# Optimization experiments

Measured on AMD Instinct MI355X. Metric: run time of the kernel, lower is better.

The kernel has to match this reference:

```python
import jax, jax.numpy as jnp
import numpy as np

DIM = 256
WIN = 4
HEADS = 4
HEAD_DIM = DIM // HEADS
SCALE = HEAD_DIM ** (-0.5)


def setup_inputs() -> dict:
    key = jax.random.key(0)
    k1, k2, k3 = jax.random.split(key, 3)
    x = jax.random.normal(k1, (4, DIM, 32, 32, 32), dtype=jnp.float32)
    # xavier_uniform with gain=0.02 ~ small weights; scale approximated
    w_qkv = jax.random.normal(k2, (3 * DIM, DIM), dtype=jnp.float32) * 0.02
    w_proj = jax.random.normal(k3, (DIM, DIM), dtype=jnp.float32) * 0.02
    return {"x": x, "w_qkv": w_qkv, "w_proj": w_proj}


def reference(x, w_qkv, w_proj):
    B, C, D, H, W = x.shape
    N = D * H * W
    s = round(N ** (1.0 / 3.0))  # perfect cube asserted by original module
    w = WIN
    # (B,C,D,H,W) -> (B,N,C) -> (B,s,s,s,C)
    xt = x.reshape(B, C, N).transpose(0, 2, 1).reshape(B, s, s, s, C)
    pad = (w - s % w) % w
    if pad:
        xt = jnp.pad(xt, ((0, 0), (0, pad), (0, pad), (0, pad), (0, 0)))
    Sp = s + pad
    n = Sp // w  # windows per axis
    # torch unfold layout: (B, nD, nH, nW, C, w, w, w)
    xw = xt.reshape(B, n, w, n, w, n, w, C).transpose(0, 1, 3, 5, 7, 2, 4, 6)
    # faithful to torch .view(-1, w*w*w, C): row-major reinterpret of (C,w,w,w)
    xw = xw.reshape(-1, w * w * w, C)  # (nw, 64, C)
    nw, ntok = xw.shape[0], xw.shape[1]
    qkv = (xw @ w_qkv.T).reshape(nw, ntok, 3, HEADS, HEAD_DIM)
    q, k, v = qkv[:, :, 0], qkv[:, :, 1], qkv[:, :, 2]  # (nw, ntok, heads, hd)
    # faithful: NO head permute in original -> attention over the heads axis
    attn = jnp.einsum('wnhd,wngd->wnhg', q, k) * SCALE  # (nw, ntok, heads, heads)
    attn = jnp.clip(attn, -10.0, 10.0)
    attn = jax.nn.softmax(attn, axis=-1)
    out = jnp.einsum('wnhg,wngd->wnhd', attn, v)  # (nw, ntok, heads, hd)
    # faithful torch transpose(1,2).reshape(nw, ntok, dim)
    out = out.transpose(0, 2, 1, 3).reshape(nw, ntok, C)
    out = out @ w_proj.T
    out = out.reshape(B, n, n, n, w, w, w, C)
    out = out.transpose(0, 1, 4, 2, 5, 3, 6, 7).reshape(B, Sp, Sp, Sp, C)
    out = out[:, :s, :s, :s, :].transpose(0, 4, 1, 2, 3)  # (B,C,s,s,s)
    return out
```

## Files before the change

### kernel.cpp

```cpp
#include <hip/hip_runtime.h>

typedef _Float16 f16;
typedef f16 f16x2 __attribute__((ext_vector_type(2)));
typedef f16 f16x4 __attribute__((ext_vector_type(4)));
typedef f16 f16x8 __attribute__((ext_vector_type(8)));
typedef float f32x4 __attribute__((ext_vector_type(4)));

union v8split { f16x8 v8; f16x2 v2[4]; };

#define WQF_OFF 0
#define WPF_OFF (768 * 256 * 2)
#define XW_OFF  (WPF_OFF + 256 * 256 * 2)
#define O2_OFF  (XW_OFF + (size_t)2048 * 16384 * 2)
#define WS_NEED (O2_OFF + (size_t)2048 * 16384 * 2)

#define QKV_LDS_OFF 32768
#define SMEM_TOTAL 131072

__global__ __launch_bounds__(256) void cvt_weights_frag_k(
    const float* __restrict__ wq, const float* __restrict__ wp,
    f16* __restrict__ wq_f, f16* __restrict__ wp_f) {
  int tid2 = blockIdx.x * 256 + threadIdx.x;
  if (tid2 < 24576) {
    const int lane = tid2 & 63, kt = (tid2 >> 6) & 7, f0 = tid2 >> 9;
    const float* s = wq + (size_t)(f0 * 16 + (lane & 15)) * 256 + kt * 32 + (lane >> 4) * 8;
    f16* d = wq_f + (size_t)tid2 * 8;
#pragma unroll
    for (int e = 0; e < 8; ++e) d[e] = (f16)s[e];
  } else if (tid2 < 32768) {
    const int t2 = tid2 - 24576;
    const int lane = t2 & 63, kt = (t2 >> 6) & 7, f0 = t2 >> 9;
    const float* s = wp + (size_t)(f0 * 16 + (lane & 15)) * 256 + kt * 32 + (lane >> 4) * 8;
    f16* d = wp_f + (size_t)t2 * 8;
#pragma unroll
    for (int e = 0; e < 8; ++e) d[e] = (f16)s[e];
  }
}

__device__ __forceinline__ char* xwp(char* s, int row, int colbyte) {
  return s + row * 512 + (colbyte ^ (((row ^ (row >> 3)) & 7) << 4));
}
__device__ __forceinline__ char* qvp(char* s, int t, int fbyte) {
  return s + QKV_LDS_OFF + t * 1536 + (fbyte ^ ((t & 7) << 4));
}

__device__ __forceinline__ float qswap1f(float v) {
  int x = __builtin_bit_cast(int, v);
  x = __builtin_amdgcn_update_dpp(0, x, 0xB1, 0xf, 0xf, true);
  return __builtin_bit_cast(float, x);
}
__device__ __forceinline__ float qswap2f(float v) {
  int x = __builtin_bit_cast(int, v);
  x = __builtin_amdgcn_update_dpp(0, x, 0x4E, 0xf, 0xf, true);
  return __builtin_bit_cast(float, x);
}

#if __has_builtin(__builtin_amdgcn_fdot2)
__device__ __forceinline__ float fdot2f(f16x2 a, f16x2 b, float c) {
  return __builtin_amdgcn_fdot2(a, b, c, false);
}
#else
__device__ __forceinline__ float fdot2f(f16x2 a, f16x2 b, float c) {
  return c + (float)a[0] * (float)b[0] + (float)a[1] * (float)b[1];
}
#endif

__global__ __launch_bounds__(256) void gather_k(const float* __restrict__ x,
                                                f16* __restrict__ xw_all) {
  const int g = blockIdx.x >> 4, cb = blockIdx.x & 15;
  const int b = g >> 6, iw = (g >> 3) & 7, jw = g & 7;
  const int tid = threadIdx.x;
  const int c = cb * 16 + (tid >> 4), a = (tid >> 2) & 3, bb = tid & 3;
  const float* src = x + (size_t)b * 8388608 + (size_t)c * 32768 +
                     (iw * 4 + a) * 1024 + (jw * 4 + bb) * 32;
  const int t = c >> 2;
  const int c2b = (c & 3) * 128 + a * 32 + bb * 8;
  const int byt = t * 512 + (c2b ^ (((t ^ (t >> 3)) & 7) << 4));
  char* wbase = (char*)(xw_all + (size_t)(g << 3) * 16384) + byt;
#pragma unroll
  for (int kw = 0; kw < 8; ++kw) {
    float4 v = *(const float4*)(src + kw * 4);
    f16x4 h;
    h[0] = (f16)v.x; h[1] = (f16)v.y; h[2] = (f16)v.z; h[3] = (f16)v.w;
    *(f16x4*)(wbase + kw * 32768) = h;
  }
}

__global__ __launch_bounds__(1024) void win_attn_k(
    const f16* __restrict__ xw_all, const f16* __restrict__ wq_f,
    const f16* __restrict__ wp_f, f16* __restrict__ o2T) {
  extern __shared__ char smem[];
  const int wi = blockIdx.x;
  const int tid = threadIdx.x, wv = tid >> 6, lane = tid & 63;
  const int lcol = lane & 15, lq = lane >> 4;

  {
    const char* g = (const char*)(xw_all + (size_t)wi * 16384) + tid * 16;
    __builtin_amdgcn_global_load_lds(
        (const __attribute__((address_space(1))) void*)(g),
        (__attribute__((address_space(3))) void*)(smem + tid * 16), 16, 0, 0);
    __builtin_amdgcn_global_load_lds(
        (const __attribute__((address_space(1))) void*)(g + 16384),
        (__attribute__((address_space(3))) void*)(smem + tid * 16 + 16384), 16, 0, 0);
  }
  __syncthreads();

  {
    f32x4 acc[3][4] = {};
    const f16* wbase = wq_f + ((size_t)wv * 3 * 8 + 0) * 64 * 8 + lane * 8;
#pragma unroll
    for (int kt = 0; kt < 8; ++kt) {
      f16x8 bf[4];
#pragma unroll
      for (int nt = 0; nt < 4; ++nt)
        bf[nt] = *(const f16x8*)xwp(smem, nt * 16 + lcol, kt * 64 + lq * 16);
#pragma unroll
      for (int ms = 0; ms < 3; ++ms) {
        f16x8 af = *(const f16x8*)(wbase + (size_t)(ms * 8 + kt) * 512);
#pragma unroll
        for (int nt = 0; nt < 4; ++nt)
          acc[ms][nt] = __builtin_amdgcn_mfma_f32_16x16x32_f16(af, bf[nt], acc[ms][nt], 0, 0, 0);
      }
    }
    const int fs = wv * 48;
#pragma unroll
    for (int ms = 0; ms < 3; ++ms)
#pragma unroll
      for (int nt = 0; nt < 4; ++nt) {
        f16x4 hv;
        hv[0] = (f16)acc[ms][nt][0]; hv[1] = (f16)acc[ms][nt][1];
        hv[2] = (f16)acc[ms][nt][2]; hv[3] = (f16)acc[ms][nt][3];
        *(f16x4*)qvp(smem, nt * 16 + lcol, (fs + ms * 16 + lq * 4) * 2) = hv;
      }
  }
  __syncthreads();

  {
    const int tt = lane >> 4, h = (lane >> 2) & 3, dq = lane & 3;
    const int t = wv * 4 + tt;
    const int db = dq * 32;

    f16x2 q2[8];
#pragma unroll
    for (int j = 0; j < 2; ++j) {
      v8split u;
      u.v8 = *(const f16x8*)qvp(smem, t, h * 128 + db + j * 16);
      q2[j * 4 + 0] = u.v2[0]; q2[j * 4 + 1] = u.v2[1];
      q2[j * 4 + 2] = u.v2[2]; q2[j * 4 + 3] = u.v2[3];
    }
    float s[4];
#pragma unroll
    for (int g = 0; g < 4; ++g) {
      float a = 0.f;
#pragma unroll
      for (int j = 0; j < 2; ++j) {
        v8split u;
        u.v8 = *(const f16x8*)qvp(smem, t, 512 + g * 128 + db + j * 16);
        a = fdot2f(q2[j * 4 + 0], u.v2[0], a);
        a = fdot2f(q2[j * 4 + 1], u.v2[1], a);
        a = fdot2f(q2[j * 4 + 2], u.v2[2], a);
        a = fdot2f(q2[j * 4 + 3], u.v2[3], a);
      }
      s[g] = a;
    }
#pragma unroll
    for (int g = 0; g < 4; ++g) {
      s[g] += qswap1f(s[g]);
      s[g] += qswap2f(s[g]);
    }

    float mx = -1e30f;
#pragma unroll
    for (int g = 0; g < 4; ++g) {
      float v = fminf(fmaxf(s[g] * 0.125f, -10.f), 10.f);
      s[g] = v; mx = fmaxf(mx, v);
    }
    float sum = 0.f;
#pragma unroll
    for (int g = 0; g < 4; ++g) { s[g] = __expf(s[g] - mx); sum += s[g]; }
    float inv = 1.f / sum;
#pragma unroll
    for (int g = 0; g < 4; ++g) s[g] *= inv;

    float o[16] = {};
#pragma unroll
    for (int g = 0; g < 4; ++g) {
      float p = s[g];
#pragma unroll
      for (int j = 0; j < 2; ++j) {
        v8split u;
        u.v8 = *(const f16x8*)qvp(smem, t, 1024 + g * 128 + db + j * 16);
#pragma unroll
        for (int i = 0; i < 4; ++i) {
          o[j * 8 + 2 * i]     += p * (float)u.v2[i][0];
          o[j * 8 + 2 * i + 1] += p * (float)u.v2[i][1];
        }
      }
    }
    const int row = h * 16 + (t >> 2);
    const int cb0 = (t & 3) * 128 + db;
#pragma unroll
    for (int j = 0; j < 2; ++j) {
      f16x8 ov;
      ov[0] = (f16)o[j * 8 + 0]; ov[1] = (f16)o[j * 8 + 1];
      ov[2] = (f16)o[j * 8 + 2]; ov[3] = (f16)o[j * 8 + 3];
      ov[4] = (f16)o[j * 8 + 4]; ov[5] = (f16)o[j * 8 + 5];
      ov[6] = (f16)o[j * 8 + 6]; ov[7] = (f16)o[j * 8 + 7];
      *(f16x8*)xwp(smem, row, cb0 + j * 16) = ov;
    }
  }
  __syncthreads();

  {
    f32x4 acc2[4] = {};
    const int c3 = wv * 16 + lcol;
    const f16* bp = wp_f + ((size_t)wv * 8) * 64 * 8 + lane * 8;
#pragma unroll
    for (int kt = 0; kt < 8; ++kt) {
      f16x8 bfr = *(const f16x8*)(bp + (size_t)kt * 512);
#pragma unroll
      for (int mt = 0; mt < 4; ++mt) {
        f16x8 afr = *(const f16x8*)xwp(smem, mt * 16 + lcol, kt * 64 + lq * 16);
        acc2[mt] = __builtin_amdgcn_mfma_f32_16x16x32_f16(afr, bfr, acc2[mt], 0, 0, 0);
      }
    }
    f16* ob = o2T + (size_t)wi * 16384;
#pragma unroll
    for (int mt = 0; mt < 4; ++mt) {
      f16x4 hv;
      hv[0] = (f16)acc2[mt][0]; hv[1] = (f16)acc2[mt][1];
      hv[2] = (f16)acc2[mt][2]; hv[3] = (f16)acc2[mt][3];
      *(f16x4*)(ob + c3 * 64 + mt * 16 + lq * 4) = hv;
    }
  }
}

__global__ __launch_bounds__(256) void scatter_k(const f16* __restrict__ o2T,
                                                 float* __restrict__ out) {
  const int g = blockIdx.x >> 4, cb = blockIdx.x & 15;
  const int b = g >> 6, iw = (g >> 3) & 7, jw = g & 7;
  const int tid = threadIdx.x;
  const int c3 = cb * 16 + (tid >> 4), a = (tid >> 2) & 3, bb = tid & 3;
  const f16* rbase = o2T + (size_t)(g << 3) * 16384 + c3 * 64 + a * 16 + bb * 4;
  float* dst = out + (size_t)b * 8388608 + (size_t)c3 * 32768 +
               (iw * 4 + a) * 1024 + (jw * 4 + bb) * 32;
#pragma unroll
  for (int kw = 0; kw < 8; ++kw) {
    f16x4 h = *(const f16x4*)(rbase + kw * 16384);
    float4 v;
    v.x = (float)h[0]; v.y = (float)h[1]; v.z = (float)h[2]; v.w = (float)h[3];
    *(float4*)(dst + kw * 4) = v;
  }
}

extern "C" void kernel_launch(void* const* d_in, const int* in_sizes, int n_in,
                              void* d_out, int out_size, void* d_ws, size_t ws_size,
                              hipStream_t stream) {
  const float* x = (const float*)d_in[0];
  const float* wq = (const float*)d_in[1];
  const float* wp = (const float*)d_in[2];
  float* out = (float*)d_out;
  char* ws = (char*)d_ws;
  f16* wq_f = (f16*)(ws + WQF_OFF);
  f16* wp_f = (f16*)(ws + WPF_OFF);
  f16* xw_all = (f16*)(ws + XW_OFF);
  f16* o2T = (f16*)(ws + O2_OFF);

  (void)hipFuncSetAttribute((const void*)win_attn_k,
                            hipFuncAttributeMaxDynamicSharedMemorySize, SMEM_TOTAL);

  cvt_weights_frag_k<<<128, 256, 0, stream>>>(wq, wp, wq_f, wp_f);
  gather_k<<<4096, 256, 0, stream>>>(x, xw_all);
  win_attn_k<<<2048, 1024, SMEM_TOTAL, stream>>>(xw_all, wq_f, wp_f, o2T);
  scatter_k<<<4096, 256, 0, stream>>>(o2T, out);
}
```

Baseline: 224.2 us.

## Fuse gather and scatter into window attention kernel, reading x and writing out directly

Removes the separate gather and scatter kernels and their fp16 workspace intermediates. The attention kernel now loads its window tile straight from the fp32 input, converts it to fp16 into LDS, and writes fp32 results directly to the output layout. This removes a round trip of two 64MB fp16 buffers and two kernel launches. In exchange, the per-block global accesses are strided 16-byte pieces and no longer use async global-to-LDS loads, which may reduce coalescing and latency hiding inside the main kernel.

```diff
diff --git a/kernel.cpp b/kernel.cpp
--- a/kernel.cpp
+++ b/kernel.cpp
@@ -10,9 +10,7 @@
 
 #define WQF_OFF 0
 #define WPF_OFF (768 * 256 * 2)
-#define XW_OFF  (WPF_OFF + 256 * 256 * 2)
-#define O2_OFF  (XW_OFF + (size_t)2048 * 16384 * 2)
-#define WS_NEED (O2_OFF + (size_t)2048 * 16384 * 2)
+#define WS_NEED (WPF_OFF + 256 * 256 * 2)
 
 #define QKV_LDS_OFF 32768
 #define SMEM_TOTAL 131072
@@ -65,49 +63,33 @@
 }
 #endif
 
-__global__ __launch_bounds__(256) void gather_k(const float* __restrict__ x,
-                                                f16* __restrict__ xw_all) {
-  const int g = blockIdx.x >> 4, cb = blockIdx.x & 15;
-  const int b = g >> 6, iw = (g >> 3) & 7, jw = g & 7;
-  const int tid = threadIdx.x;
-  const int c = cb * 16 + (tid >> 4), a = (tid >> 2) & 3, bb = tid & 3;
-  const float* src = x + (size_t)b * 8388608 + (size_t)c * 32768 +
-                     (iw * 4 + a) * 1024 + (jw * 4 + bb) * 32;
-  const int t = c >> 2;
-  const int c2b = (c & 3) * 128 + a * 32 + bb * 8;
-  const int byt = t * 512 + (c2b ^ (((t ^ (t >> 3)) & 7) << 4));
-  char* wbase = (char*)(xw_all + (size_t)(g << 3) * 16384) + byt;
-#pragma unroll
-  for (int kw = 0; kw < 8; ++kw) {
-    float4 v = *(const float4*)(src + kw * 4);
-    f16x4 h;
-    h[0] = (f16)v.x; h[1] = (f16)v.y; h[2] = (f16)v.z; h[3] = (f16)v.w;
-    *(f16x4*)(wbase + kw * 32768) = h;
-  }
-}
-
-__global__ __launch_bounds__(1024) void win_attn_k(
-    const f16* __restrict__ xw_all, const f16* __restrict__ wq_f,
-    const f16* __restrict__ wp_f, f16* __restrict__ o2T) {
+__global__ __launch_bounds__(1024) void win_k(
+    const float* __restrict__ x, const f16* __restrict__ wq_f,
+    const f16* __restrict__ wp_f, float* __restrict__ out) {
   extern __shared__ char smem[];
-  const int wi = blockIdx.x;
+  const int blk = blockIdx.x;
+  const int slab = blk & 255, kw = blk >> 8;
+  const int b = slab >> 6, zi = (slab >> 3) & 7, yj = slab & 7;
   const int tid = threadIdx.x, wv = tid >> 6, lane = tid & 63;
   const int lcol = lane & 15, lq = lane >> 4;
 
   {
-    const char* g = (const char*)(xw_all + (size_t)wi * 16384) + tid * 16;
-    __builtin_amdgcn_global_load_lds(
-        (const __attribute__((address_space(1))) void*)(g),
-        (__attribute__((address_space(3))) void*)(smem + tid * 16), 16, 0, 0);
-    __builtin_amdgcn_global_load_lds(
-        (const __attribute__((address_space(1))) void*)(g + 16384),
-        (__attribute__((address_space(3))) void*)(smem + tid * 16 + 16384), 16, 0, 0);
+    const float* xb = x + (size_t)b * 8388608 + zi * 4096 + yj * 128 + kw * 4;
+#pragma unroll
+    for (int it = 0; it < 4; ++it) {
+      int idx = it * 1024 + tid;
+      int c = idx >> 4, a = (idx >> 2) & 3, bb = idx & 3;
+      float4 v = *(const float4*)(xb + (size_t)c * 32768 + a * 1024 + bb * 32);
+      f16x4 h;
+      h[0] = (f16)v.x; h[1] = (f16)v.y; h[2] = (f16)v.z; h[3] = (f16)v.w;
+      *(f16x4*)xwp(smem, c >> 2, (c & 3) * 128 + a * 32 + bb * 8) = h;
+    }
   }
   __syncthreads();
 
   {
     f32x4 acc[3][4] = {};
-    const f16* wbase = wq_f + ((size_t)wv * 3 * 8 + 0) * 64 * 8 + lane * 8;
+    const f16* wbase = wq_f + ((size_t)wv * 3 * 8) * 64 * 8 + lane * 8;
 #pragma unroll
     for (int kt = 0; kt < 8; ++kt) {
       f16x8 bf[4];
@@ -224,32 +206,14 @@
         acc2[mt] = __builtin_amdgcn_mfma_f32_16x16x32_f16(afr, bfr, acc2[mt], 0, 0, 0);
       }
     }
-    f16* ob = o2T + (size_t)wi * 16384;
+    float* ob = out + (size_t)b * 8388608 + zi * 4096 + yj * 128 + kw * 4;
 #pragma unroll
     for (int mt = 0; mt < 4; ++mt) {
-      f16x4 hv;
-      hv[0] = (f16)acc2[mt][0]; hv[1] = (f16)acc2[mt][1];
-      hv[2] = (f16)acc2[mt][2]; hv[3] = (f16)acc2[mt][3];
-      *(f16x4*)(ob + c3 * 64 + mt * 16 + lq * 4) = hv;
-    }
-  }
-}
-
-__global__ __launch_bounds__(256) void scatter_k(const f16* __restrict__ o2T,
-                                                 float* __restrict__ out) {
-  const int g = blockIdx.x >> 4, cb = blockIdx.x & 15;
-  const int b = g >> 6, iw = (g >> 3) & 7, jw = g & 7;
-  const int tid = threadIdx.x;
-  const int c3 = cb * 16 + (tid >> 4), a = (tid >> 2) & 3, bb = tid & 3;
-  const f16* rbase = o2T + (size_t)(g << 3) * 16384 + c3 * 64 + a * 16 + bb * 4;
-  float* dst = out + (size_t)b * 8388608 + (size_t)c3 * 32768 +
-               (iw * 4 + a) * 1024 + (jw * 4 + bb) * 32;
-#pragma unroll
-  for (int kw = 0; kw < 8; ++kw) {
-    f16x4 h = *(const f16x4*)(rbase + kw * 16384);
-    float4 v;
-    v.x = (float)h[0]; v.y = (float)h[1]; v.z = (float)h[2]; v.w = (float)h[3];
-    *(float4*)(dst + kw * 4) = v;
+      float4 v;
+      v.x = acc2[mt][0]; v.y = acc2[mt][1];
+      v.z = acc2[mt][2]; v.w = acc2[mt][3];
+      *(float4*)(ob + (size_t)c3 * 32768 + mt * 1024 + lq * 32) = v;
+    }
   }
 }
 
@@ -263,14 +227,10 @@
   char* ws = (char*)d_ws;
   f16* wq_f = (f16*)(ws + WQF_OFF);
   f16* wp_f = (f16*)(ws + WPF_OFF);
-  f16* xw_all = (f16*)(ws + XW_OFF);
-  f16* o2T = (f16*)(ws + O2_OFF);
-
-  (void)hipFuncSetAttribute((const void*)win_attn_k,
+
+  (void)hipFuncSetAttribute((const void*)win_k,
                             hipFuncAttributeMaxDynamicSharedMemorySize, SMEM_TOTAL);
 
   cvt_weights_frag_k<<<128, 256, 0, stream>>>(wq, wp, wq_f, wp_f);
-  gather_k<<<4096, 256, 0, stream>>>(x, xw_all);
-  win_attn_k<<<2048, 1024, SMEM_TOTAL, stream>>>(xw_all, wq_f, wp_f, o2T);
-  scatter_k<<<4096, 256, 0, stream>>>(o2T, out);
-}
+  win_k<<<2048, 1024, SMEM_TOTAL, stream>>>(x, wq_f, wp_f, out);
+}
```

New measurement: 325.7 us. +45.2%, slower.

## Split each window's attention block into two half-window blocks with half the LDS

Applied to the files above, without the earlier changes.

Each window's work moves from one 1024-thread block into two 512-thread blocks, each handling half the token rows; the gather layout is re-indexed so each half is contiguous. LDS per block drops from 128KB to 64KB so more blocks can be resident per CU and loads can overlap with compute. The trade-off is that each block reloads the full QKV and projection weight fragments, which doubles weight traffic, and the output store pattern is remapped.

```diff
diff --git a/kernel.cpp b/kernel.cpp
--- a/kernel.cpp
+++ b/kernel.cpp
@@ -14,8 +14,8 @@
 #define O2_OFF  (XW_OFF + (size_t)2048 * 16384 * 2)
 #define WS_NEED (O2_OFF + (size_t)2048 * 16384 * 2)
 
-#define QKV_LDS_OFF 32768
-#define SMEM_TOTAL 131072
+#define QKV_LDS_OFF 16384
+#define SMEM_TOTAL 65536
 
 __global__ __launch_bounds__(256) void cvt_weights_frag_k(
     const float* __restrict__ wq, const float* __restrict__ wp,
@@ -73,60 +73,62 @@
   const int c = cb * 16 + (tid >> 4), a = (tid >> 2) & 3, bb = tid & 3;
   const float* src = x + (size_t)b * 8388608 + (size_t)c * 32768 +
                      (iw * 4 + a) * 1024 + (jw * 4 + bb) * 32;
-  const int t = c >> 2;
+  const int t = c >> 2, hb = t >> 5, tl = t & 31;
   const int c2b = (c & 3) * 128 + a * 32 + bb * 8;
-  const int byt = t * 512 + (c2b ^ (((t ^ (t >> 3)) & 7) << 4));
-  char* wbase = (char*)(xw_all + (size_t)(g << 3) * 16384) + byt;
+  const int byt = tl * 512 + (c2b ^ (((tl ^ (tl >> 3)) & 7) << 4));
+  char* wbase = (char*)(xw_all + (size_t)(g * 16 + hb) * 8192) + byt;
 #pragma unroll
   for (int kw = 0; kw < 8; ++kw) {
     float4 v = *(const float4*)(src + kw * 4);
     f16x4 h;
     h[0] = (f16)v.x; h[1] = (f16)v.y; h[2] = (f16)v.z; h[3] = (f16)v.w;
-    *(f16x4*)(wbase + kw * 32768) = h;
-  }
-}
-
-__global__ __launch_bounds__(1024) void win_attn_k(
+    *(f16x4*)(wbase + (size_t)kw * 32768) = h;
+  }
+}
+
+__global__ __launch_bounds__(512) void win_attn_k(
     const f16* __restrict__ xw_all, const f16* __restrict__ wq_f,
     const f16* __restrict__ wp_f, f16* __restrict__ o2T) {
   extern __shared__ char smem[];
-  const int wi = blockIdx.x;
+  const int hw = blockIdx.x;
+  const int wi = hw >> 1, hb = hw & 1;
   const int tid = threadIdx.x, wv = tid >> 6, lane = tid & 63;
   const int lcol = lane & 15, lq = lane >> 4;
 
   {
-    const char* g = (const char*)(xw_all + (size_t)wi * 16384) + tid * 16;
-    __builtin_amdgcn_global_load_lds(
-        (const __attribute__((address_space(1))) void*)(g),
-        (__attribute__((address_space(3))) void*)(smem + tid * 16), 16, 0, 0);
-    __builtin_amdgcn_global_load_lds(
-        (const __attribute__((address_space(1))) void*)(g + 16384),
-        (__attribute__((address_space(3))) void*)(smem + tid * 16 + 16384), 16, 0, 0);
+    const char* g = (const char*)(xw_all + (size_t)hw * 8192) + tid * 16;
+#pragma unroll
+    for (int i = 0; i < 2; ++i)
+      __builtin_amdgcn_global_load_lds(
+          (const __attribute__((address_space(1))) void*)(g + i * 8192),
+          (__attribute__((address_space(3))) void*)(smem + tid * 16 + i * 8192),
+          16, 0, 0);
   }
   __syncthreads();
 
-  {
-    f32x4 acc[3][4] = {};
-    const f16* wbase = wq_f + ((size_t)wv * 3 * 8 + 0) * 64 * 8 + lane * 8;
+#pragma unroll 1
+  for (int half = 0; half < 2; ++half) {
+    f32x4 acc[3][2] = {};
+    const f16* wbase = wq_f + (size_t)(wv * 6 + half * 3) * 8 * 512 + lane * 8;
 #pragma unroll
     for (int kt = 0; kt < 8; ++kt) {
-      f16x8 bf[4];
-#pragma unroll
-      for (int nt = 0; nt < 4; ++nt)
+      f16x8 bf[2];
+#pragma unroll
+      for (int nt = 0; nt < 2; ++nt)
         bf[nt] = *(const f16x8*)xwp(smem, nt * 16 + lcol, kt * 64 + lq * 16);
 #pragma unroll
       for (int ms = 0; ms < 3; ++ms) {
         f16x8 af = *(const f16x8*)(wbase + (size_t)(ms * 8 + kt) * 512);
 #pragma unroll
-        for (int nt = 0; nt < 4; ++nt)
+        for (int nt = 0; nt < 2; ++nt)
           acc[ms][nt] = __builtin_amdgcn_mfma_f32_16x16x32_f16(af, bf[nt], acc[ms][nt], 0, 0, 0);
       }
     }
-    const int fs = wv * 48;
+    const int fs = wv * 96 + half * 48;
 #pragma unroll
     for (int ms = 0; ms < 3; ++ms)
 #pragma unroll
-      for (int nt = 0; nt < 4; ++nt) {
+      for (int nt = 0; nt < 2; ++nt) {
         f16x4 hv;
         hv[0] = (f16)acc[ms][nt][0]; hv[1] = (f16)acc[ms][nt][1];
         hv[2] = (f16)acc[ms][nt][2]; hv[3] = (f16)acc[ms][nt][3];
@@ -137,14 +139,14 @@
 
   {
     const int tt = lane >> 4, h = (lane >> 2) & 3, dq = lane & 3;
-    const int t = wv * 4 + tt;
+    const int tl = wv * 4 + tt;
     const int db = dq * 32;
 
     f16x2 q2[8];
 #pragma unroll
     for (int j = 0; j < 2; ++j) {
       v8split u;
-      u.v8 = *(const f16x8*)qvp(smem, t, h * 128 + db + j * 16);
+      u.v8 = *(const f16x8*)qvp(smem, tl, h * 128 + db + j * 16);
       q2[j * 4 + 0] = u.v2[0]; q2[j * 4 + 1] = u.v2[1];
       q2[j * 4 + 2] = u.v2[2]; q2[j * 4 + 3] = u.v2[3];
     }
@@ -155,7 +157,7 @@
 #pragma unroll
       for (int j = 0; j < 2; ++j) {
         v8split u;
-        u.v8 = *(const f16x8*)qvp(smem, t, 512 + g * 128 + db + j * 16);
+        u.v8 = *(const f16x8*)qvp(smem, tl, 512 + g * 128 + db + j * 16);
         a = fdot2f(q2[j * 4 + 0], u.v2[0], a);
         a = fdot2f(q2[j * 4 + 1], u.v2[1], a);
         a = fdot2f(q2[j * 4 + 2], u.v2[2], a);
@@ -189,7 +191,7 @@
 #pragma unroll
       for (int j = 0; j < 2; ++j) {
         v8split u;
-        u.v8 = *(const f16x8*)qvp(smem, t, 1024 + g * 128 + db + j * 16);
+        u.v8 = *(const f16x8*)qvp(smem, tl, 1024 + g * 128 + db + j * 16);
 #pragma unroll
         for (int i = 0; i < 4; ++i) {
           o[j * 8 + 2 * i]     += p * (float)u.v2[i][0];
@@ -197,8 +199,8 @@
         }
       }
     }
-    const int row = h * 16 + (t >> 2);
-    const int cb0 = (t & 3) * 128 + db;
+    const int row = h * 8 + (tl >> 2);
+    const int cb0 = (tl & 3) * 128 + db;
 #pragma unroll
     for (int j = 0; j < 2; ++j) {
       f16x8 ov;
@@ -212,26 +214,35 @@
   __syncthreads();
 
   {
-    f32x4 acc2[4] = {};
-    const int c3 = wv * 16 + lcol;
-    const f16* bp = wp_f + ((size_t)wv * 8) * 64 * 8 + lane * 8;
+    f32x4 acc2[2][2] = {};
 #pragma unroll
     for (int kt = 0; kt < 8; ++kt) {
-      f16x8 bfr = *(const f16x8*)(bp + (size_t)kt * 512);
-#pragma unroll
-      for (int mt = 0; mt < 4; ++mt) {
-        f16x8 afr = *(const f16x8*)xwp(smem, mt * 16 + lcol, kt * 64 + lq * 16);
-        acc2[mt] = __builtin_amdgcn_mfma_f32_16x16x32_f16(afr, bfr, acc2[mt], 0, 0, 0);
+      f16x8 afr[2];
+#pragma unroll
+      for (int mt = 0; mt < 2; ++mt)
+        afr[mt] = *(const f16x8*)xwp(smem, mt * 16 + lcol, kt * 64 + lq * 16);
+#pragma unroll
+      for (int nt = 0; nt < 2; ++nt) {
+        f16x8 bfr = *(const f16x8*)(wp_f + (size_t)(wv * 2 + nt) * 8 * 512 +
+                                    (size_t)kt * 512 + lane * 8);
+#pragma unroll
+        for (int mt = 0; mt < 2; ++mt)
+          acc2[mt][nt] = __builtin_amdgcn_mfma_f32_16x16x32_f16(afr[mt], bfr, acc2[mt][nt], 0, 0, 0);
       }
     }
     f16* ob = o2T + (size_t)wi * 16384;
-#pragma unroll
-    for (int mt = 0; mt < 4; ++mt) {
-      f16x4 hv;
-      hv[0] = (f16)acc2[mt][0]; hv[1] = (f16)acc2[mt][1];
-      hv[2] = (f16)acc2[mt][2]; hv[3] = (f16)acc2[mt][3];
-      *(f16x4*)(ob + c3 * 64 + mt * 16 + lq * 4) = hv;
-    }
+    const int t2b = hb * 8 + ((lq & 1) * 4);
+#pragma unroll
+    for (int mt = 0; mt < 2; ++mt)
+#pragma unroll
+      for (int nt = 0; nt < 2; ++nt) {
+        int c3 = wv * 32 + nt * 16 + lcol;
+        int t2 = (mt * 2 + (lq >> 1)) * 16 + t2b;
+        f16x4 hv;
+        hv[0] = (f16)acc2[mt][nt][0]; hv[1] = (f16)acc2[mt][nt][1];
+        hv[2] = (f16)acc2[mt][nt][2]; hv[3] = (f16)acc2[mt][nt][3];
+        *(f16x4*)(ob + c3 * 64 + t2) = hv;
+      }
   }
 }
 
@@ -271,6 +282,6 @@
 
   cvt_weights_frag_k<<<128, 256, 0, stream>>>(wq, wp, wq_f, wp_f);
   gather_k<<<4096, 256, 0, stream>>>(x, xw_all);
-  win_attn_k<<<2048, 1024, SMEM_TOTAL, stream>>>(xw_all, wq_f, wp_f, o2T);
+  win_attn_k<<<4096, 512, SMEM_TOTAL, stream>>>(xw_all, wq_f, wp_f, o2T);
   scatter_k<<<4096, 256, 0, stream>>>(o2T, out);
 }
```

Result: slower. 233.1 us (+3.9%).

## Make attention blocks persistent over eight windows with double-buffered LDS prefetch

Applied to the files above, without the earlier changes.

The attention kernel now launches 256 blocks instead of 2048, and each block loops over eight windows. While the attention math for the current window runs, the next window's input tile is loaded asynchronously from global memory straight into a second LDS buffer. This is meant to hide global-load latency and to save per-block launch and ramp-up cost. In exchange, LDS use per block grows to 160KB, and correctness depends on the barriers also making the asynchronous LDS loads complete before the buffer is read.

```diff
diff --git a/kernel.cpp b/kernel.cpp
--- a/kernel.cpp
+++ b/kernel.cpp
@@ -14,8 +14,8 @@
 #define O2_OFF  (XW_OFF + (size_t)2048 * 16384 * 2)
 #define WS_NEED (O2_OFF + (size_t)2048 * 16384 * 2)
 
-#define QKV_LDS_OFF 32768
-#define SMEM_TOTAL 131072
+#define QKV_LDS_OFF 65536
+#define SMEM_TOTAL 163840
 
 __global__ __launch_bounds__(256) void cvt_weights_frag_k(
     const float* __restrict__ wq, const float* __restrict__ wp,
@@ -90,30 +90,31 @@
     const f16* __restrict__ xw_all, const f16* __restrict__ wq_f,
     const f16* __restrict__ wp_f, f16* __restrict__ o2T) {
   extern __shared__ char smem[];
-  const int wi = blockIdx.x;
+  const int blk = blockIdx.x;
   const int tid = threadIdx.x, wv = tid >> 6, lane = tid & 63;
   const int lcol = lane & 15, lq = lane >> 4;
-
-  {
-    const char* g = (const char*)(xw_all + (size_t)wi * 16384) + tid * 16;
+  char* buf0 = smem;
+  char* buf1 = smem + 32768;
+
+  auto PREF = [&](int w, char* buf) {
+    const char* g = (const char*)(xw_all + (size_t)(blk * 8 + w) * 16384) + tid * 16;
     __builtin_amdgcn_global_load_lds(
         (const __attribute__((address_space(1))) void*)(g),
-        (__attribute__((address_space(3))) void*)(smem + tid * 16), 16, 0, 0);
+        (__attribute__((address_space(3))) void*)(buf + tid * 16), 16, 0, 0);
     __builtin_amdgcn_global_load_lds(
         (const __attribute__((address_space(1))) void*)(g + 16384),
-        (__attribute__((address_space(3))) void*)(smem + tid * 16 + 16384), 16, 0, 0);
-  }
-  __syncthreads();
-
-  {
+        (__attribute__((address_space(3))) void*)(buf + tid * 16 + 16384), 16, 0, 0);
+  };
+
+  auto G1 = [&](char* buf) {
     f32x4 acc[3][4] = {};
-    const f16* wbase = wq_f + ((size_t)wv * 3 * 8 + 0) * 64 * 8 + lane * 8;
+    const f16* wbase = wq_f + ((size_t)wv * 3 * 8) * 64 * 8 + lane * 8;
 #pragma unroll
     for (int kt = 0; kt < 8; ++kt) {
       f16x8 bf[4];
 #pragma unroll
       for (int nt = 0; nt < 4; ++nt)
-        bf[nt] = *(const f16x8*)xwp(smem, nt * 16 + lcol, kt * 64 + lq * 16);
+        bf[nt] = *(const f16x8*)xwp(buf, nt * 16 + lcol, kt * 64 + lq * 16);
 #pragma unroll
       for (int ms = 0; ms < 3; ++ms) {
         f16x8 af = *(const f16x8*)(wbase + (size_t)(ms * 8 + kt) * 512);
@@ -132,10 +133,9 @@
         hv[2] = (f16)acc[ms][nt][2]; hv[3] = (f16)acc[ms][nt][3];
         *(f16x4*)qvp(smem, nt * 16 + lcol, (fs + ms * 16 + lq * 4) * 2) = hv;
       }
-  }
-  __syncthreads();
-
-  {
+  };
+
+  auto ATTN = [&](char* buf) {
     const int tt = lane >> 4, h = (lane >> 2) & 3, dq = lane & 3;
     const int t = wv * 4 + tt;
     const int db = dq * 32;
@@ -206,12 +206,11 @@
       ov[2] = (f16)o[j * 8 + 2]; ov[3] = (f16)o[j * 8 + 3];
       ov[4] = (f16)o[j * 8 + 4]; ov[5] = (f16)o[j * 8 + 5];
       ov[6] = (f16)o[j * 8 + 6]; ov[7] = (f16)o[j * 8 + 7];
-      *(f16x8*)xwp(smem, row, cb0 + j * 16) = ov;
-    }
-  }
-  __syncthreads();
-
-  {
+      *(f16x8*)xwp(buf, row, cb0 + j * 16) = ov;
+    }
+  };
+
+  auto G2 = [&](char* buf, int w) {
     f32x4 acc2[4] = {};
     const int c3 = wv * 16 + lcol;
     const f16* bp = wp_f + ((size_t)wv * 8) * 64 * 8 + lane * 8;
@@ -220,11 +219,11 @@
       f16x8 bfr = *(const f16x8*)(bp + (size_t)kt * 512);
 #pragma unroll
       for (int mt = 0; mt < 4; ++mt) {
-        f16x8 afr = *(const f16x8*)xwp(smem, mt * 16 + lcol, kt * 64 + lq * 16);
+        f16x8 afr = *(const f16x8*)xwp(buf, mt * 16 + lcol, kt * 64 + lq * 16);
         acc2[mt] = __builtin_amdgcn_mfma_f32_16x16x32_f16(afr, bfr, acc2[mt], 0, 0, 0);
       }
     }
-    f16* ob = o2T + (size_t)wi * 16384;
+    f16* ob = o2T + (size_t)(blk * 8 + w) * 16384;
 #pragma unroll
     for (int mt = 0; mt < 4; ++mt) {
       f16x4 hv;
@@ -232,6 +231,20 @@
       hv[2] = (f16)acc2[mt][2]; hv[3] = (f16)acc2[mt][3];
       *(f16x4*)(ob + c3 * 64 + mt * 16 + lq * 4) = hv;
     }
+  };
+
+  PREF(0, buf0);
+  __syncthreads();
+#pragma unroll 1
+  for (int w = 0; w < 8; ++w) {
+    char* cur = (w & 1) ? buf1 : buf0;
+    char* nxt = (w & 1) ? buf0 : buf1;
+    G1(cur);
+    __syncthreads();
+    if (w < 7) PREF(w + 1, nxt);
+    ATTN(cur);
+    __syncthreads();
+    G2(cur, w);
   }
 }
 
@@ -271,6 +284,6 @@
 
   cvt_weights_frag_k<<<128, 256, 0, stream>>>(wq, wp, wq_f, wp_f);
   gather_k<<<4096, 256, 0, stream>>>(x, xw_all);
-  win_attn_k<<<2048, 1024, SMEM_TOTAL, stream>>>(xw_all, wq_f, wp_f, o2T);
+  win_attn_k<<<256, 1024, SMEM_TOTAL, stream>>>(xw_all, wq_f, wp_f, o2T);
   scatter_k<<<4096, 256, 0, stream>>>(o2T, out);
 }
```

New measurement: 427.2 us. 1.91x slower.
